# Kernel optimization log

Hardware: AMD Instinct MI355X
Metric: run time of the kernel (lower is better)

Reference implementation:

```python
import jax, jax.numpy as jnp
from jax import lax
import numpy as np

B, N, H, K = 64, 256, 1024, 3  # batch, num_proposals, hidden_dim, conv kernel size
LN_EPS = 1e-5


def setup_inputs() -> dict:
    key = jax.random.key(0)
    k1, k2, k3 = jax.random.split(key, 3)
    scale = 1.0 / np.sqrt(H)
    return {
        "f": jax.random.normal(k1, (B, N, H), dtype=jnp.float32),
        "k": jax.random.normal(k2, (B, N, H), dtype=jnp.float32),
        "W_lin": jax.random.normal(k3, (N * K, H), dtype=jnp.float32) * scale,
        "b_lin": jnp.zeros((N * K,), dtype=jnp.float32),
        "ln_gamma": jnp.ones((H,), dtype=jnp.float32),
        "ln_beta": jnp.zeros((H,), dtype=jnp.float32),
    }


def _conv_one(x, w):
    # x: [N, H] (channels, length); w: [N_out, N_in, K]
    # PyTorch F.conv1d is cross-correlation, same as lax conv with no flip.
    y = lax.conv_general_dilated(
        x[None], w, window_strides=(1,), padding="SAME",
        dimension_numbers=("NCH", "OIH", "NCH"))
    return y[0]  # [N, H]


def reference(f, k, W_lin, b_lin, ln_gamma, ln_beta):
    # Dynamic weight generation: [B, N, H] -> [B, N, N*K] -> [B, N, N, K]
    weight = jnp.einsum("bnh,oh->bno", f, W_lin) + b_lin
    weight = weight.reshape(B, N, N, K)
    # Per-sample dynamic conv1d over the hidden dim (batched via vmap)
    out = jax.vmap(_conv_one)(k, weight)  # [B, N, H]
    # LayerNorm over hidden dim
    mu = jnp.mean(out, axis=-1, keepdims=True)
    var = jnp.var(out, axis=-1, keepdims=True)
    out = (out - mu) * lax.rsqrt(var + LN_EPS) * ln_gamma + ln_beta
    return out
```

## Files before the change

### kernel.cpp

```cpp
#include <hip/hip_runtime.h>
#include <math.h>

#define Bsz 64
#define Nn  256
#define Hh  1024
#define NK  768

typedef __bf16 bf16;
typedef bf16 bf16x4 __attribute__((ext_vector_type(4)));
typedef bf16 bf16x8 __attribute__((ext_vector_type(8)));
typedef float floatx4 __attribute__((ext_vector_type(4)));

#define KT_ROWS   1026
#define KT_BSTRIDE (KT_ROWS * 256)

__device__ __forceinline__ void gl_lds16(const bf16* g, bf16* l) {
    __builtin_amdgcn_global_load_lds(
        (__attribute__((address_space(1))) void*)(g),
        (__attribute__((address_space(3))) void*)(l), 16, 0, 0);
}

__device__ __forceinline__ bf16x8 cvt8(float4 a, float4 b) {
    bf16x8 v;
    v[0] = (bf16)a.x; v[1] = (bf16)a.y; v[2] = (bf16)a.z; v[3] = (bf16)a.w;
    v[4] = (bf16)b.x; v[5] = (bf16)b.y; v[6] = (bf16)b.z; v[7] = (bf16)b.w;
    return v;
}

__global__ __launch_bounds__(256) void prep_gemm_kernel(
    const float* __restrict__ A32,
    const float* __restrict__ W32,
    const float* __restrict__ bias,
    const float* __restrict__ kin,
    bf16* __restrict__ wgt3,
    bf16* __restrict__ kTp)
{
    __shared__ bf16 smem[14336];
    const int tid = threadIdx.x;

    if (blockIdx.x >= 1024) {
        int id = blockIdx.x - 1024;
        int hb = id & 15, ib = (id >> 4) & 3, b = id >> 6;
        int i0 = ib * 64, h0 = hb * 64;
        const float* src = kin + ((size_t)b << 18);
        bf16* dstb = kTp + (size_t)b * KT_BSTRIDE;
        bf16* T = smem;

        if (hb == 0 && ib == 0) {
            dstb[tid] = (bf16)0.f;
            dstb[(size_t)1025 * 256 + tid] = (bf16)0.f;
        }
        #pragma unroll
        for (int j = 0; j < 4; ++j) {
            int s = tid + j * 256;
            int il = s >> 4, c4 = s & 15;
            float4 v = *(const float4*)&src[(size_t)(i0 + il) * Hh + h0 + c4 * 4];
            T[(c4 * 4 + 0) * 72 + il] = (bf16)v.x;
            T[(c4 * 4 + 1) * 72 + il] = (bf16)v.y;
            T[(c4 * 4 + 2) * 72 + il] = (bf16)v.z;
            T[(c4 * 4 + 3) * 72 + il] = (bf16)v.w;
        }
        __syncthreads();
        #pragma unroll
        for (int p = 0; p < 2; ++p) {
            int hl = (tid >> 3) + p * 32;
            int q  = tid & 7;
            bf16x8 v = *(const bf16x8*)&T[hl * 72 + q * 8];
            *(bf16x8*)&dstb[(size_t)(h0 + hl + 1) * 256 + i0 + q * 8] = v;
        }
        return;
    }

    bf16* As = smem;
    bf16* Bs = smem + 8192;
    const int wave = tid >> 6, lane = tid & 63;
    const int row0 = (blockIdx.x >> 3) * 128;
    const int col0 = (blockIdx.x & 7) * 96;

    const float* gA[4]; bf16* lA[4];
    #pragma unroll
    for (int j = 0; j < 4; ++j) {
        int s = tid + j * 256;
        int reg = s >> 9, rem = s & 511, row = rem >> 2, quad = rem & 3;
        gA[j] = A32 + (size_t)(row0 + row) * Hh + reg * 32 + quad * 8;
        lA[j] = As + s * 8;
    }
    const float* gB[3]; bf16* lB[3];
    #pragma unroll
    for (int j = 0; j < 3; ++j) {
        int s = tid + j * 256;
        int reg = s / 384, rem = s - reg * 384, row = rem >> 2, quad = rem & 3;
        gB[j] = W32 + (size_t)(col0 + row) * Hh + reg * 32 + quad * 8;
        lB[j] = Bs + s * 8;
    }

    const int wm = wave & 1, wn = wave >> 1;
    const int fm = lane & 15, koct = (lane >> 4) * 8;

    floatx4 zero = {0.f, 0.f, 0.f, 0.f};
    floatx4 acc[4][3];
    #pragma unroll
    for (int i = 0; i < 4; ++i)
        #pragma unroll
        for (int j = 0; j < 3; ++j) acc[i][j] = zero;

    for (int k0 = 0; k0 < Hh; k0 += 64) {
        float4 av[4][2], bv[3][2];
        #pragma unroll
        for (int j = 0; j < 4; ++j) {
            av[j][0] = ((const float4*)(gA[j] + k0))[0];
            av[j][1] = ((const float4*)(gA[j] + k0))[1];
        }
        #pragma unroll
        for (int j = 0; j < 3; ++j) {
            bv[j][0] = ((const float4*)(gB[j] + k0))[0];
            bv[j][1] = ((const float4*)(gB[j] + k0))[1];
        }
        __syncthreads();
        #pragma unroll
        for (int j = 0; j < 4; ++j) *(bf16x8*)lA[j] = cvt8(av[j][0], av[j][1]);
        #pragma unroll
        for (int j = 0; j < 3; ++j) *(bf16x8*)lB[j] = cvt8(bv[j][0], bv[j][1]);
        __syncthreads();
        #pragma unroll
        for (int q = 0; q < 2; ++q) {
            bf16x8 af[4], bfr[3];
            #pragma unroll
            for (int mt = 0; mt < 4; ++mt)
                af[mt] = *(const bf16x8*)&As[q * 4096 + (wm * 64 + mt * 16 + fm) * 32 + koct];
            #pragma unroll
            for (int nt = 0; nt < 3; ++nt)
                bfr[nt] = *(const bf16x8*)&Bs[q * 3072 + (wn * 48 + nt * 16 + fm) * 32 + koct];
            #pragma unroll
            for (int mt = 0; mt < 4; ++mt)
                #pragma unroll
                for (int nt = 0; nt < 3; ++nt)
                    acc[mt][nt] = __builtin_amdgcn_mfma_f32_16x16x32_bf16(
                        af[mt], bfr[nt], acc[mt][nt], 0, 0, 0);
        }
    }
    __syncthreads();

    const int b  = row0 >> 8;
    const int nb = row0 & 255;
    bf16* Cs = smem;
    #pragma unroll
    for (int nt = 0; nt < 3; ++nt) {
        int c = wn * 48 + nt * 16 + fm;
        float bl = bias[col0 + c];
        #pragma unroll
        for (int mt = 0; mt < 4; ++mt) {
            int rb = wm * 64 + mt * 16 + (lane >> 4) * 4;
            #pragma unroll
            for (int r = 0; r < 4; ++r)
                Cs[(rb + r) * 104 + c] = (bf16)(acc[mt][nt][r] + bl);
        }
    }
    __syncthreads();
    const int i0 = (blockIdx.x & 7) * 32;
    #pragma unroll
    for (int j = 0; j < 6; ++j) {
        int s = tid + j * 256;
        int t = s / 512, rem = s & 511, n = rem >> 2, q8 = rem & 3;
        bf16x8 v;
        #pragma unroll
        for (int u = 0; u < 8; ++u)
            v[u] = Cs[n * 104 + (q8 * 8 + u) * 3 + t];
        *(bf16x8*)&wgt3[((size_t)(b * 3 + t) << 16) + ((size_t)(nb + n) << 8) + i0 + q8 * 8] = v;
    }
}

__global__ __launch_bounds__(256, 3) void conv_mfma(
    const bf16* __restrict__ kTp,
    const bf16* __restrict__ wgt3,
    float* __restrict__ out)
{
    __shared__ bf16 As[6144];
    __shared__ bf16 Ks[8256];
    const int tid  = threadIdx.x;
    const int wave = tid >> 6, lane = tid & 63;
    const int b  = blockIdx.z;
    const int o0 = blockIdx.y * 64;
    const int h0 = blockIdx.x * 256;
    const int wm = wave & 1, wn = wave >> 1;
    const int fm = lane & 15, koct = (lane >> 4) * 8;

    const bf16* gA[3]; bf16* lA[3];
    #pragma unroll
    for (int j = 0; j < 3; ++j) {
        int s = tid + j * 256;
        int t = s >> 8, rem = s & 255, o = rem >> 2, iq = rem & 3;
        gA[j] = wgt3 + ((size_t)(b * 3 + t) << 16) + ((size_t)(o0 + o) << 8) + iq * 8;
        lA[j] = As + s * 8;
    }
    const bf16* kb = kTp + (size_t)b * KT_BSTRIDE;
    const bf16* gK[4]; bf16* lK[4];
    #pragma unroll
    for (int j = 0; j < 4; ++j) {
        int s = tid + j * 256;
        int r = s >> 2, quad = s & 3;
        gK[j] = kb + (size_t)(h0 + r) * 256 + quad * 8;
        lK[j] = Ks + s * 8;
    }

    floatx4 zero = {0.f, 0.f, 0.f, 0.f};
    floatx4 acc[2][8];
    #pragma unroll
    for (int i = 0; i < 2; ++i)
        #pragma unroll
        for (int j = 0; j < 8; ++j) acc[i][j] = zero;

    for (int ic = 0; ic < 8; ++ic) {
        const int i0 = ic * 32;
        __syncthreads();
        #pragma unroll
        for (int j = 0; j < 3; ++j) gl_lds16(gA[j] + i0, lA[j]);
        #pragma unroll
        for (int j = 0; j < 4; ++j) gl_lds16(gK[j] + i0, lK[j]);
        if (tid < 8) {
            int r = 256 + (tid >> 2), q = tid & 3;
            bf16x8 v = *(const bf16x8*)&kb[(size_t)(h0 + r) * 256 + i0 + q * 8];
            *(bf16x8*)&Ks[r * 32 + q * 8] = v;
        }
        __syncthreads();
        #pragma unroll
        for (int t = 0; t < 3; ++t) {
            bf16x8 af[2], bfr[8];
            #pragma unroll
            for (int mt = 0; mt < 2; ++mt)
                af[mt] = *(const bf16x8*)&As[t * 2048 + (wm * 32 + mt * 16 + fm) * 32 + koct];
            #pragma unroll
            for (int nt = 0; nt < 8; ++nt)
                bfr[nt] = *(const bf16x8*)&Ks[(wn * 128 + nt * 16 + fm + t) * 32 + koct];
            #pragma unroll
            for (int mt = 0; mt < 2; ++mt)
                #pragma unroll
                for (int nt = 0; nt < 8; ++nt)
                    acc[mt][nt] = __builtin_amdgcn_mfma_f32_16x16x32_bf16(
                        af[mt], bfr[nt], acc[mt][nt], 0, 0, 0);
        }
    }

    #pragma unroll
    for (int mt = 0; mt < 2; ++mt) {
        int o = o0 + wm * 32 + mt * 16 + (lane >> 4) * 4;
        #pragma unroll
        for (int nt = 0; nt < 8; ++nt) {
            int h = h0 + wn * 128 + nt * 16 + fm;
            #pragma unroll
            for (int r = 0; r < 4; ++r)
                out[((size_t)(b * 256 + o + r) << 10) + h] = acc[mt][nt][r];
        }
    }
}

__global__ __launch_bounds__(256) void ln_kernel(
    float* __restrict__ io, const float* __restrict__ gamma,
    const float* __restrict__ beta)
{
    const int row = blockIdx.x;
    const int tid = threadIdx.x;
    float* p = io + ((size_t)row << 10);
    float4 v = ((const float4*)p)[tid];
    float x[4] = {v.x, v.y, v.z, v.w};
    float s1 = x[0] + x[1] + x[2] + x[3];
    float s2 = x[0]*x[0] + x[1]*x[1] + x[2]*x[2] + x[3]*x[3];
    #pragma unroll
    for (int m = 1; m < 64; m <<= 1) {
        s1 += __shfl_xor(s1, m, 64);
        s2 += __shfl_xor(s2, m, 64);
    }
    __shared__ float r1[4], r2[4];
    if ((tid & 63) == 0) { r1[tid >> 6] = s1; r2[tid >> 6] = s2; }
    __syncthreads();
    float S1 = r1[0] + r1[1] + r1[2] + r1[3];
    float S2 = r2[0] + r2[1] + r2[2] + r2[3];
    float mu   = S1 * (1.0f / 1024.0f);
    float var  = S2 * (1.0f / 1024.0f) - mu * mu;
    float rstd = rsqrtf(var + 1e-5f);
    float4 g  = ((const float4*)gamma)[tid];
    float4 be = ((const float4*)beta)[tid];
    float4 o;
    o.x = (x[0] - mu) * rstd * g.x + be.x;
    o.y = (x[1] - mu) * rstd * g.y + be.y;
    o.z = (x[2] - mu) * rstd * g.z + be.z;
    o.w = (x[3] - mu) * rstd * g.w + be.w;
    ((float4*)p)[tid] = o;
}

extern "C" void kernel_launch(void* const* d_in, const int* in_sizes, int n_in,
                              void* d_out, int out_size, void* d_ws, size_t ws_size,
                              hipStream_t stream) {
    const float* f     = (const float*)d_in[0];
    const float* kin   = (const float*)d_in[1];
    const float* W_lin = (const float*)d_in[2];
    const float* b_lin = (const float*)d_in[3];
    const float* gamma = (const float*)d_in[4];
    const float* beta  = (const float*)d_in[5];
    float* out = (float*)d_out;

    char* ws = (char*)d_ws;
    bf16* kTp  = (bf16*)(ws);
    bf16* wgt3 = (bf16*)(ws + 33619968);

    prep_gemm_kernel<<<5120, 256, 0, stream>>>(f, W_lin, b_lin, kin, wgt3, kTp);
    conv_mfma<<<dim3(4, 4, 64), 256, 0, stream>>>(kTp, wgt3, out);
    ln_kernel<<<16384, 256, 0, stream>>>(out, gamma, beta);
}
```

Baseline: 300.6 us.

## Pre-convert GEMM inputs to bf16, use direct-to-LDS loads, bf16 conv output

Splits the fused prep+GEMM kernel in two. A prep kernel first converts f and W_lin to bf16 alongside the k transpose. The GEMM then streams bf16 tiles with global_load_lds and uses a wider 192-column tile per block. The conv kernel now writes bf16 into a scratch buffer (aliased over the consumed fbf region), and the LayerNorm reads it and writes fp32 output. This trades an extra launch and an extra pass over f for less GEMM load traffic and smaller intermediate write/read, at some precision cost before LayerNorm.

```diff
diff --git a/kernel.cpp b/kernel.cpp
--- a/kernel.cpp
+++ b/kernel.cpp
@@ -20,77 +20,87 @@
         (__attribute__((address_space(3))) void*)(l), 16, 0, 0);
 }
 
-__device__ __forceinline__ bf16x8 cvt8(float4 a, float4 b) {
-    bf16x8 v;
-    v[0] = (bf16)a.x; v[1] = (bf16)a.y; v[2] = (bf16)a.z; v[3] = (bf16)a.w;
-    v[4] = (bf16)b.x; v[5] = (bf16)b.y; v[6] = (bf16)b.z; v[7] = (bf16)b.w;
-    return v;
-}
-
-__global__ __launch_bounds__(256) void prep_gemm_kernel(
-    const float* __restrict__ A32,
-    const float* __restrict__ W32,
+__global__ __launch_bounds__(256) void prep_kernel(
+    const float* __restrict__ f, const float* __restrict__ wl,
+    const float* __restrict__ kin,
+    bf16* __restrict__ fbf, bf16* __restrict__ wlbf, bf16* __restrict__ kTp)
+{
+    __shared__ bf16 T[64 * 72];
+    const int tid = threadIdx.x;
+    const int bid = blockIdx.x;
+
+    if (bid < 16384) {
+        int i = bid * 256 + tid;
+        float4 v = ((const float4*)f)[i];
+        bf16x4 o = { (bf16)v.x, (bf16)v.y, (bf16)v.z, (bf16)v.w };
+        ((bf16x4*)fbf)[i] = o;
+        return;
+    }
+    if (bid < 17152) {
+        int j = (bid - 16384) * 256 + tid;
+        float4 v = ((const float4*)wl)[j];
+        bf16x4 o = { (bf16)v.x, (bf16)v.y, (bf16)v.z, (bf16)v.w };
+        ((bf16x4*)wlbf)[j] = o;
+        return;
+    }
+    int id = bid - 17152;
+    int hb = id & 15, ib = (id >> 4) & 3, b = id >> 6;
+    int i0 = ib * 64, h0 = hb * 64;
+    const float* src = kin + ((size_t)b << 18);
+    bf16* dstb = kTp + (size_t)b * KT_BSTRIDE;
+
+    if (hb == 0 && ib == 0) {
+        dstb[tid] = (bf16)0.f;
+        dstb[(size_t)1025 * 256 + tid] = (bf16)0.f;
+    }
+    #pragma unroll
+    for (int j = 0; j < 4; ++j) {
+        int s = tid + j * 256;
+        int il = s >> 4, c4 = s & 15;
+        float4 v = *(const float4*)&src[(size_t)(i0 + il) * Hh + h0 + c4 * 4];
+        T[(c4 * 4 + 0) * 72 + il] = (bf16)v.x;
+        T[(c4 * 4 + 1) * 72 + il] = (bf16)v.y;
+        T[(c4 * 4 + 2) * 72 + il] = (bf16)v.z;
+        T[(c4 * 4 + 3) * 72 + il] = (bf16)v.w;
+    }
+    __syncthreads();
+    #pragma unroll
+    for (int p = 0; p < 2; ++p) {
+        int hl = (tid >> 3) + p * 32;
+        int q  = tid & 7;
+        bf16x8 v = *(const bf16x8*)&T[hl * 72 + q * 8];
+        *(bf16x8*)&dstb[(size_t)(h0 + hl + 1) * 256 + i0 + q * 8] = v;
+    }
+}
+
+__global__ __launch_bounds__(256) void gemm1_mfma(
+    const bf16* __restrict__ A,
+    const bf16* __restrict__ Bw,
     const float* __restrict__ bias,
-    const float* __restrict__ kin,
-    bf16* __restrict__ wgt3,
-    bf16* __restrict__ kTp)
+    bf16* __restrict__ wgt3)
 {
-    __shared__ bf16 smem[14336];
-    const int tid = threadIdx.x;
-
-    if (blockIdx.x >= 1024) {
-        int id = blockIdx.x - 1024;
-        int hb = id & 15, ib = (id >> 4) & 3, b = id >> 6;
-        int i0 = ib * 64, h0 = hb * 64;
-        const float* src = kin + ((size_t)b << 18);
-        bf16* dstb = kTp + (size_t)b * KT_BSTRIDE;
-        bf16* T = smem;
-
-        if (hb == 0 && ib == 0) {
-            dstb[tid] = (bf16)0.f;
-            dstb[(size_t)1025 * 256 + tid] = (bf16)0.f;
-        }
-        #pragma unroll
-        for (int j = 0; j < 4; ++j) {
-            int s = tid + j * 256;
-            int il = s >> 4, c4 = s & 15;
-            float4 v = *(const float4*)&src[(size_t)(i0 + il) * Hh + h0 + c4 * 4];
-            T[(c4 * 4 + 0) * 72 + il] = (bf16)v.x;
-            T[(c4 * 4 + 1) * 72 + il] = (bf16)v.y;
-            T[(c4 * 4 + 2) * 72 + il] = (bf16)v.z;
-            T[(c4 * 4 + 3) * 72 + il] = (bf16)v.w;
-        }
-        __syncthreads();
-        #pragma unroll
-        for (int p = 0; p < 2; ++p) {
-            int hl = (tid >> 3) + p * 32;
-            int q  = tid & 7;
-            bf16x8 v = *(const bf16x8*)&T[hl * 72 + q * 8];
-            *(bf16x8*)&dstb[(size_t)(h0 + hl + 1) * 256 + i0 + q * 8] = v;
-        }
-        return;
-    }
-
+    __shared__ bf16 smem[25600];
     bf16* As = smem;
     bf16* Bs = smem + 8192;
+    const int tid  = threadIdx.x;
     const int wave = tid >> 6, lane = tid & 63;
-    const int row0 = (blockIdx.x >> 3) * 128;
-    const int col0 = (blockIdx.x & 7) * 96;
-
-    const float* gA[4]; bf16* lA[4];
+    const int row0 = blockIdx.y * 128;
+    const int col0 = blockIdx.x * 192;
+
+    const bf16* gA[4]; bf16* lA[4];
     #pragma unroll
     for (int j = 0; j < 4; ++j) {
         int s = tid + j * 256;
         int reg = s >> 9, rem = s & 511, row = rem >> 2, quad = rem & 3;
-        gA[j] = A32 + (size_t)(row0 + row) * Hh + reg * 32 + quad * 8;
+        gA[j] = A + (size_t)(row0 + row) * Hh + reg * 32 + quad * 8;
         lA[j] = As + s * 8;
     }
-    const float* gB[3]; bf16* lB[3];
-    #pragma unroll
-    for (int j = 0; j < 3; ++j) {
-        int s = tid + j * 256;
-        int reg = s / 384, rem = s - reg * 384, row = rem >> 2, quad = rem & 3;
-        gB[j] = W32 + (size_t)(col0 + row) * Hh + reg * 32 + quad * 8;
+    const bf16* gB[6]; bf16* lB[6];
+    #pragma unroll
+    for (int j = 0; j < 6; ++j) {
+        int s = tid + j * 256;
+        int reg = s / 768, rem = s - reg * 768, row = rem >> 2, quad = rem & 3;
+        gB[j] = Bw + (size_t)(col0 + row) * Hh + reg * 32 + quad * 8;
         lB[j] = Bs + s * 8;
     }
 
@@ -98,74 +108,62 @@
     const int fm = lane & 15, koct = (lane >> 4) * 8;
 
     floatx4 zero = {0.f, 0.f, 0.f, 0.f};
-    floatx4 acc[4][3];
+    floatx4 acc[4][6];
     #pragma unroll
     for (int i = 0; i < 4; ++i)
         #pragma unroll
-        for (int j = 0; j < 3; ++j) acc[i][j] = zero;
+        for (int j = 0; j < 6; ++j) acc[i][j] = zero;
 
     for (int k0 = 0; k0 < Hh; k0 += 64) {
-        float4 av[4][2], bv[3][2];
-        #pragma unroll
-        for (int j = 0; j < 4; ++j) {
-            av[j][0] = ((const float4*)(gA[j] + k0))[0];
-            av[j][1] = ((const float4*)(gA[j] + k0))[1];
-        }
-        #pragma unroll
-        for (int j = 0; j < 3; ++j) {
-            bv[j][0] = ((const float4*)(gB[j] + k0))[0];
-            bv[j][1] = ((const float4*)(gB[j] + k0))[1];
-        }
+        #pragma unroll
+        for (int j = 0; j < 4; ++j) gl_lds16(gA[j] + k0, lA[j]);
+        #pragma unroll
+        for (int j = 0; j < 6; ++j) gl_lds16(gB[j] + k0, lB[j]);
         __syncthreads();
         #pragma unroll
-        for (int j = 0; j < 4; ++j) *(bf16x8*)lA[j] = cvt8(av[j][0], av[j][1]);
-        #pragma unroll
-        for (int j = 0; j < 3; ++j) *(bf16x8*)lB[j] = cvt8(bv[j][0], bv[j][1]);
-        __syncthreads();
-        #pragma unroll
         for (int q = 0; q < 2; ++q) {
-            bf16x8 af[4], bfr[3];
+            bf16x8 af[4], bfr[6];
             #pragma unroll
             for (int mt = 0; mt < 4; ++mt)
                 af[mt] = *(const bf16x8*)&As[q * 4096 + (wm * 64 + mt * 16 + fm) * 32 + koct];
             #pragma unroll
-            for (int nt = 0; nt < 3; ++nt)
-                bfr[nt] = *(const bf16x8*)&Bs[q * 3072 + (wn * 48 + nt * 16 + fm) * 32 + koct];
+            for (int nt = 0; nt < 6; ++nt)
+                bfr[nt] = *(const bf16x8*)&Bs[q * 6144 + (wn * 96 + nt * 16 + fm) * 32 + koct];
             #pragma unroll
             for (int mt = 0; mt < 4; ++mt)
                 #pragma unroll
-                for (int nt = 0; nt < 3; ++nt)
+                for (int nt = 0; nt < 6; ++nt)
                     acc[mt][nt] = __builtin_amdgcn_mfma_f32_16x16x32_bf16(
                         af[mt], bfr[nt], acc[mt][nt], 0, 0, 0);
         }
-    }
-    __syncthreads();
+        __syncthreads();
+    }
 
     const int b  = row0 >> 8;
     const int nb = row0 & 255;
     bf16* Cs = smem;
     #pragma unroll
-    for (int nt = 0; nt < 3; ++nt) {
-        int c = wn * 48 + nt * 16 + fm;
+    for (int nt = 0; nt < 6; ++nt) {
+        int c = wn * 96 + nt * 16 + fm;
         float bl = bias[col0 + c];
         #pragma unroll
         for (int mt = 0; mt < 4; ++mt) {
             int rb = wm * 64 + mt * 16 + (lane >> 4) * 4;
             #pragma unroll
             for (int r = 0; r < 4; ++r)
-                Cs[(rb + r) * 104 + c] = (bf16)(acc[mt][nt][r] + bl);
+                Cs[(rb + r) * 200 + c] = (bf16)(acc[mt][nt][r] + bl);
         }
     }
     __syncthreads();
-    const int i0 = (blockIdx.x & 7) * 32;
-    #pragma unroll
-    for (int j = 0; j < 6; ++j) {
-        int s = tid + j * 256;
-        int t = s / 512, rem = s & 511, n = rem >> 2, q8 = rem & 3;
+    const int i0 = blockIdx.x * 64;
+    #pragma unroll
+    for (int j = 0; j < 12; ++j) {
+        int s = tid + j * 256;
+        int t = s >> 10, rem = s & 1023, n = rem >> 3, q8 = rem & 7;
         bf16x8 v;
         #pragma unroll
         for (int u = 0; u < 8; ++u)
-            v[u] = Cs[n * 104 + (q8 * 8 + u) * 3 + t];
+            v[u] = Cs[n * 200 + (q8 * 8 + u) * 3 + t];
         *(bf16x8*)&wgt3[((size_t)(b * 3 + t) << 16) + ((size_t)(nb + n) << 8) + i0 + q8 * 8] = v;
     }
 }
@@ -173,7 +171,7 @@
 __global__ __launch_bounds__(256, 3) void conv_mfma(
     const bf16* __restrict__ kTp,
     const bf16* __restrict__ wgt3,
-    float* __restrict__ out)
+    bf16* __restrict__ cbuf)
 {
     __shared__ bf16 As[6144];
     __shared__ bf16 Ks[8256];
@@ -249,20 +247,19 @@
             int h = h0 + wn * 128 + nt * 16 + fm;
             #pragma unroll
             for (int r = 0; r < 4; ++r)
-                out[((size_t)(b * 256 + o + r) << 10) + h] = acc[mt][nt][r];
+                cbuf[((size_t)(b * 256 + o + r) << 10) + h] = (bf16)acc[mt][nt][r];
         }
     }
 }
 
 __global__ __launch_bounds__(256) void ln_kernel(
-    float* __restrict__ io, const float* __restrict__ gamma,
-    const float* __restrict__ beta)
+    const bf16* __restrict__ cbuf, const float* __restrict__ gamma,
+    const float* __restrict__ beta, float* __restrict__ out)
 {
     const int row = blockIdx.x;
     const int tid = threadIdx.x;
-    float* p = io + ((size_t)row << 10);
-    float4 v = ((const float4*)p)[tid];
-    float x[4] = {v.x, v.y, v.z, v.w};
+    bf16x4 v = ((const bf16x4*)(cbuf + ((size_t)row << 10)))[tid];
+    float x[4] = {(float)v[0], (float)v[1], (float)v[2], (float)v[3]};
     float s1 = x[0] + x[1] + x[2] + x[3];
     float s2 = x[0]*x[0] + x[1]*x[1] + x[2]*x[2] + x[3]*x[3];
     #pragma unroll
@@ -285,7 +282,7 @@
     o.y = (x[1] - mu) * rstd * g.y + be.y;
     o.z = (x[2] - mu) * rstd * g.z + be.z;
     o.w = (x[3] - mu) * rstd * g.w + be.w;
-    ((float4*)p)[tid] = o;
+    ((float4*)(out + ((size_t)row << 10)))[tid] = o;
 }
 
 extern "C" void kernel_launch(void* const* d_in, const int* in_sizes, int n_in,
@@ -300,10 +297,14 @@
     float* out = (float*)d_out;
 
     char* ws = (char*)d_ws;
-    bf16* kTp  = (bf16*)(ws);
-    bf16* wgt3 = (bf16*)(ws + 33619968);
-
-    prep_gemm_kernel<<<5120, 256, 0, stream>>>(f, W_lin, b_lin, kin, wgt3, kTp);
-    conv_mfma<<<dim3(4, 4, 64), 256, 0, stream>>>(kTp, wgt3, out);
-    ln_kernel<<<16384, 256, 0, stream>>>(out, gamma, beta);
-}
+    bf16* fbf  = (bf16*)(ws);
+    bf16* cbuf = (bf16*)(ws);
+    bf16* wlbf = (bf16*)(ws + 33554432);
+    bf16* kTp  = (bf16*)(ws + 35127296);
+    bf16* wgt3 = (bf16*)(ws + 68747264);
+
+    prep_kernel<<<21248, 256, 0, stream>>>(f, W_lin, kin, fbf, wlbf, kTp);
+    gemm1_mfma<<<dim3(4, 128), 256, 0, stream>>>(fbf, wlbf, b_lin, wgt3);
+    conv_mfma<<<dim3(4, 4, 64), 256, 0, stream>>>(kTp, wgt3, cbuf);
+    ln_kernel<<<16384, 256, 0, stream>>>(cbuf, gamma, beta, out);
+}
```

Measured after the change: 271.6 us. 9.7% less time.
